# Optimization experiments

Hardware: AMD Instinct MI355X
Metric: run time of the kernel (lower is better)

## Reference

```python
import jax, jax.numpy as jnp
import numpy as np

DIM = 1024
INTER = 512
E = 32            # n_routed_experts
TOPK = 4          # n_activated_experts
GROUPS = 8        # n_expert_groups
TOPK_GROUPS = 4
SHARED_INTER = 2 * INTER  # n_shared_experts * moe_inter_dim
ROUTE_SCALE = 1.0
B, S = 8, 4096


def setup_inputs() -> dict:
    key = jax.random.key(0)
    ks = jax.random.split(key, 16)
    def xav(k, shape):
        fan_in, fan_out = shape[-2], shape[-1]
        lim = np.sqrt(6.0 / (fan_in + fan_out))
        return jax.random.uniform(k, shape, jnp.float32, -lim, lim)
    return {
        "x": jax.random.normal(ks[0], (B, S, DIM), jnp.float32),
        "gw": xav(ks[1], (DIM, E)),
        "gb": jnp.zeros((E,), jnp.float32),
        "w1": xav(ks[2], (E, DIM, INTER)),
        "b1": jnp.zeros((E, INTER), jnp.float32),
        "w3": xav(ks[3], (E, DIM, INTER)),
        "b3": jnp.zeros((E, INTER), jnp.float32),
        "w2": xav(ks[4], (E, INTER, DIM)),
        "b2": jnp.zeros((E, DIM), jnp.float32),
        "sw1": xav(ks[5], (DIM, SHARED_INTER)),
        "sb1": jnp.zeros((SHARED_INTER,), jnp.float32),
        "sw3": xav(ks[6], (DIM, SHARED_INTER)),
        "sb3": jnp.zeros((SHARED_INTER,), jnp.float32),
        "sw2": xav(ks[7], (SHARED_INTER, DIM)),
        "sb2": jnp.zeros((DIM,), jnp.float32),
    }


def _gate(xf, gw, gb):
    # scores: softmax over routed experts in fp32 (score_func='softmax')
    T = xf.shape[0]
    scores = jax.nn.softmax((xf @ gw + gb).astype(jnp.float32), axis=-1)  # [T, E]
    original_scores = scores
    # group-masked routing (n_expert_groups > 1)
    scores_g = scores.reshape(T, GROUPS, E // GROUPS)                     # [T, G, E/G]
    group_scores = jnp.sum(jax.lax.top_k(scores_g, 2)[0], axis=-1)        # [T, G]
    gidx = jax.lax.top_k(group_scores, TOPK_GROUPS)[1]                    # [T, topk_groups]
    keep = jnp.zeros((T, GROUPS), bool).at[jnp.arange(T)[:, None], gidx].set(True)
    masked = jnp.where(keep[:, :, None], scores_g, -jnp.inf).reshape(T, E)
    indices = jax.lax.top_k(masked, TOPK)[1]                              # [T, topk]
    weights = jnp.take_along_axis(original_scores, indices, axis=1) * ROUTE_SCALE
    return weights.astype(xf.dtype), indices


def reference(x, gw, gb, w1, b1, w3, b3, w2, b2, sw1, sb1, sw3, sb3, sw2, sb2):
    shape = x.shape
    xf = x.reshape(-1, DIM)                                               # [T, dim]
    T = xf.shape[0]
    weights, indices = _gate(xf, gw, gb)
    # dense combine weights [T, E]: w_e(t) = routing weight if expert e chosen for t else 0
    cw = jnp.zeros((T, E), xf.dtype).at[jnp.arange(T)[:, None], indices].add(weights)
    # scan over experts: y += w_e * SwiGLU_e(x). Zero weight -> zero contribution,
    # identical math to the masked dispatch/scatter-add in the torch code.
    def body(y, p):
        w1e, b1e, w3e, b3e, w2e, b2e, we = p
        h = jax.nn.silu(xf @ w1e + b1e) * (xf @ w3e + b3e)                # [T, inter]
        return y + we[:, None] * (h @ w2e + b2e), None
    y0 = jnp.zeros_like(xf)
    y, _ = jax.lax.scan(body, y0, (w1, b1, w3, b3, w2, b2, cw.T))
    # shared experts MLP (SwiGLU)
    z = (jax.nn.silu(xf @ sw1 + sb1) * (xf @ sw3 + sb3)) @ sw2 + sb2
    return (y + z).reshape(shape)
```

## Files before the change

kernel.cpp:

```cpp
#include <hip/hip_runtime.h>
#include <stdint.h>

#define DIM_    1024
#define INTER_  512

typedef short bf16x4 __attribute__((ext_vector_type(4)));
typedef short bf16x8 __attribute__((ext_vector_type(8)));
typedef float f32x4  __attribute__((ext_vector_type(4)));

__device__ __forceinline__ unsigned short f2bf(float f) {
  union { float f; unsigned u; } v; v.f = f;
  return (unsigned short)((v.u + 0x7FFFu + ((v.u >> 16) & 1u)) >> 16);
}
__device__ __forceinline__ unsigned f2bf2(float a, float b) {
  union { float f; unsigned u; } va, vb; va.f = a; vb.f = b;
  unsigned ra = (va.u + 0x7FFFu + ((va.u >> 16) & 1u)) >> 16;
  unsigned rb = (vb.u + 0x7FFFu + ((vb.u >> 16) & 1u)) >> 16;
  return ra | (rb << 16);
}
__device__ __forceinline__ float bfhi(unsigned u) {
  union { unsigned u; float f; } v; v.u = u & 0xffff0000u; return v.f;
}
__device__ __forceinline__ float bflo(unsigned u) {
  union { unsigned u; float f; } v; v.u = u << 16; return v.f;
}

__device__ __forceinline__ void gl16(const void* g, void* l) {
  __builtin_amdgcn_global_load_lds(
      (const __attribute__((address_space(1))) unsigned int*)g,
      (__attribute__((address_space(3))) unsigned int*)l, 16, 0, 0);
}

__global__ __launch_bounds__(256) void gate_kernel(
    const float* __restrict__ x, const float* __restrict__ gw,
    const float* __restrict__ gb, int* __restrict__ idx, float* __restrict__ wts,
    unsigned short* __restrict__ xb) {
  __shared__ double s_sc[4][32];
  __shared__ double s_gs[4][8];
  const int wid = threadIdx.x >> 6, lane = threadIdx.x & 63;
  const int t = blockIdx.x * 4 + wid;
  {
    const float* xrow = x + (size_t)t * DIM_ + lane * 16;
    unsigned short* xbrow = xb + (size_t)t * DIM_ + lane * 16;
    float4 f0 = *(const float4*)(xrow);
    float4 f1 = *(const float4*)(xrow + 4);
    float4 f2v = *(const float4*)(xrow + 8);
    float4 f3v = *(const float4*)(xrow + 12);
    uint4 o0, o1;
    o0.x = f2bf2(f0.x, f0.y);  o0.y = f2bf2(f0.z, f0.w);
    o0.z = f2bf2(f1.x, f1.y);  o0.w = f2bf2(f1.z, f1.w);
    o1.x = f2bf2(f2v.x, f2v.y); o1.y = f2bf2(f2v.z, f2v.w);
    o1.z = f2bf2(f3v.x, f3v.y); o1.w = f2bf2(f3v.z, f3v.w);
    *(uint4*)(xbrow) = o0;
    *(uint4*)(xbrow + 8) = o1;
  }
  const int e = lane & 31, half = lane >> 5;
  const float* xr  = x  + (size_t)t * DIM_ + half * 512;
  const float* gwp = gw + (size_t)half * 512 * 32 + e;
  double a0 = 0, a1 = 0, a2 = 0, a3 = 0;
  for (int k = 0; k < 512; k += 4) {
    float4 xv = *(const float4*)(xr + k);
    a0 += (double)xv.x * (double)gwp[(k + 0) * 32];
    a1 += (double)xv.y * (double)gwp[(k + 1) * 32];
    a2 += (double)xv.z * (double)gwp[(k + 2) * 32];
    a3 += (double)xv.w * (double)gwp[(k + 3) * 32];
  }
  double lg = (a0 + a1) + (a2 + a3);
  lg += __shfl_xor(lg, 32);
  lg += (double)gb[e];
  double m = lg;
  #pragma unroll
  for (int d = 1; d < 32; d <<= 1) m = fmax(m, __shfl_xor(m, d));
  double ex = exp(lg - m);
  double ssum = ex;
  #pragma unroll
  for (int d = 1; d < 32; d <<= 1) ssum += __shfl_xor(ssum, d);
  double sc = ex / ssum;
  double p  = __shfl_xor(sc, 1);
  double m1 = fmax(sc, p), n1 = fmin(sc, p);
  double m2 = __shfl_xor(m1, 2), n2 = __shfl_xor(n1, 2);
  double gs = (m1 >= m2) ? (m1 + fmax(n1, m2)) : (m2 + fmax(n2, m1));
  if (lane < 32) {
    s_sc[wid][e] = sc;
    if ((e & 3) == 0) s_gs[wid][e >> 2] = gs;
  }
  __syncthreads();
  if (lane == 0) {
    unsigned kmask = 0;
    for (int it = 0; it < 4; ++it) {
      int bg = 0; double bv = -1.0;
      for (int g = 0; g < 8; ++g)
        if (!((kmask >> g) & 1u) && s_gs[wid][g] > bv) { bv = s_gs[wid][g]; bg = g; }
      kmask |= 1u << bg;
    }
    unsigned umask = 0;
    for (int slot = 0; slot < 4; ++slot) {
      int be = 0; double bv = -1.0;
      for (int ee = 0; ee < 32; ++ee)
        if (((kmask >> (ee >> 2)) & 1u) && !((umask >> ee) & 1u) && s_sc[wid][ee] > bv) {
          bv = s_sc[wid][ee]; be = ee;
        }
      umask |= 1u << be;
      idx[t * 4 + slot] = be;
      wts[t * 4 + slot] = (float)bv;
    }
  }
}

__global__ __launch_bounds__(256) void count_kernel(const int* __restrict__ idx,
                                                    int* __restrict__ meta) {
  __shared__ int h[32];
  int tid = threadIdx.x;
  if (tid < 32) h[tid] = 0;
  __syncthreads();
  atomicAdd(&h[idx[blockIdx.x * 256 + tid]], 1);
  __syncthreads();
  if (tid < 32 && h[tid]) atomicAdd(&meta[tid], h[tid]);
}

__global__ void scan_kernel(int* __restrict__ meta) {
  int lane = threadIdx.x & 63;
  if (lane < 32) {
    int c = meta[lane];
    int pre = c;
    #pragma unroll
    for (int d = 1; d < 32; d <<= 1) { int t = __shfl_up(pre, d); if (lane >= d) pre += t; }
    int excl = pre - c;
    meta[64 + lane] = excl;
    meta[32 + lane] = excl;
    int nt = (c + 127) >> 7;
    int ntp = nt;
    #pragma unroll
    for (int d = 1; d < 32; d <<= 1) { int t = __shfl_up(ntp, d); if (lane >= d) ntp += t; }
    int ntExcl = ntp - nt;
    for (int k = 0; k < nt; ++k) { meta[128 + ntExcl + k] = lane; meta[1184 + ntExcl + k] = k << 7; }
    if (lane == 31) { meta[96] = excl + c; meta[97] = ntExcl + nt; }
  }
}

__global__ __launch_bounds__(256) void scatter_kernel(
    const int* __restrict__ idx, int* __restrict__ meta,
    int* __restrict__ tok, int* __restrict__ inv) {
  int i = blockIdx.x * 256 + threadIdx.x;
  int lane = threadIdx.x & 63;
  int e = idx[i];
  unsigned long long m = ~0ull;
  #pragma unroll
  for (int b = 0; b < 5; ++b) {
    unsigned long long vote = __ballot((e >> b) & 1);
    m &= ((e >> b) & 1) ? vote : ~vote;
  }
  int leader = __ffsll((long long)m) - 1;
  int rank = __popcll(m & ((1ull << lane) - 1));
  int base = 0;
  if (lane == leader) base = atomicAdd(&meta[32 + e], (int)__popcll(m));
  base = __shfl(base, leader);
  int p = base + rank;
  tok[p] = i >> 2;
  inv[i] = p;
}

__global__ __launch_bounds__(256) void repack_kernel(
    const float* __restrict__ src, unsigned short* __restrict__ dst,
    int K, int N, int tilesPerMat) {
  const int w = blockIdx.x * 4 + (threadIdx.x >> 6);
  const int j = threadIdx.x & 63;
  const int e = w / tilesPerMat, rem = w % tilesPerMat;
  const int kSteps = K >> 5;
  const int nt = rem / kSteps, kq = rem % kSteps;
  const float* s = src + (size_t)e * K * N + (size_t)(kq * 32) * N + nt * 64 + j;
  float v[32];
  #pragma unroll
  for (int kk = 0; kk < 32; ++kk) v[kk] = s[(size_t)kk * N];
  char* d = (char*)dst + (size_t)w * 4096 + j * 64;
  const int sz = (j & 3) ^ ((j >> 2) & 3);
  #pragma unroll
  for (int q = 0; q < 4; ++q) {
    int o = (q ^ sz) * 8;
    uint4 tv;
    tv.x = f2bf2(v[o + 0], v[o + 1]);
    tv.y = f2bf2(v[o + 2], v[o + 3]);
    tv.z = f2bf2(v[o + 4], v[o + 5]);
    tv.w = f2bf2(v[o + 6], v[o + 7]);
    *(uint4*)(d + q * 16) = tv;
  }
}

__global__ __launch_bounds__(256) void s1_kernel(
    const unsigned short* __restrict__ xb, const unsigned short* __restrict__ b1i,
    const unsigned short* __restrict__ b3i, const float* __restrict__ sb1,
    const float* __restrict__ sb3, unsigned short* __restrict__ Hs) {
  __shared__ char lds[32768];
  const int n0 = blockIdx.x * 64;
  const int m0 = blockIdx.y * 128;
  const int tid = threadIdx.x, lane = tid & 63, wave = tid >> 6;
  const int wm = wave >> 1, wn = wave & 1;

  const int r0 = tid >> 2, s0 = tid & 3;
  const int vrw = (r0 & 3) ^ ((r0 >> 2) & 1);
  const char* a0 = (const char*)xb + (size_t)(m0 + r0) * 2048 + ((s0 ^ vrw) << 4);
  const char* a1 = (const char*)xb + (size_t)(m0 + r0 + 64) * 2048 + ((s0 ^ vrw) << 4);
  const char* b1p = (const char*)b1i + (size_t)(blockIdx.x * 32) * 4096 + tid * 16;
  const char* b3p = (const char*)b3i + (size_t)(blockIdx.x * 32) * 4096 + tid * 16;

  const int g = lane >> 4;
  const int vfr = (lane & 3) ^ ((lane >> 2) & 1);
  const int aro = (wm * 64 + (lane & 15)) * 64 + ((g ^ vfr) << 4);
  int bofs[2];
  #pragma unroll
  for (int ni = 0; ni < 2; ++ni) {
    int j = wn * 32 + ni * 16 + (lane & 15);
    int sz = (j & 3) ^ ((j >> 2) & 3);
    bofs[ni] = j * 64 + ((g ^ sz) << 4);
  }

  f32x4 acc1[4][2], acc3[4][2];
  const f32x4 zz = {0.f, 0.f, 0.f, 0.f};
  #pragma unroll
  for (int mi = 0; mi < 4; ++mi)
    #pragma unroll
    for (int ni = 0; ni < 2; ++ni) { acc1[mi][ni] = zz; acc3[mi][ni] = zz; }

  auto stage = [&](int buf, int kq) {
    char* b = lds + buf * 16384;
    gl16(a0 + kq * 64, b + wave * 1024);
    gl16(a1 + kq * 64, b + 4096 + wave * 1024);
    gl16(b1p + (size_t)kq * 4096, b + 8192 + wave * 1024);
    gl16(b3p + (size_t)kq * 4096, b + 12288 + wave * 1024);
  };
  stage(0, 0);
  __syncthreads();
  int cur = 0;
  for (int kq = 0; kq < 32; ++kq) {
    if (kq + 1 < 32) stage(cur ^ 1, kq + 1);
    char* cb = lds + cur * 16384;
    bf16x8 af[4];
    #pragma unroll
    for (int mi = 0; mi < 4; ++mi) af[mi] = *(const bf16x8*)(cb + aro + mi * 1024);
    #pragma unroll
    for (int ni = 0; ni < 2; ++ni) {
      bf16x8 bv = *(const bf16x8*)(cb + 8192 + bofs[ni]);
      #pragma unroll
      for (int mi = 0; mi < 4; ++mi)
        acc1[mi][ni] = __builtin_amdgcn_mfma_f32_16x16x32_bf16(af[mi], bv, acc1[mi][ni], 0, 0, 0);
      bf16x8 bv3 = *(const bf16x8*)(cb + 12288 + bofs[ni]);
      #pragma unroll
      for (int mi = 0; mi < 4; ++mi)
        acc3[mi][ni] = __builtin_amdgcn_mfma_f32_16x16x32_bf16(af[mi], bv3, acc3[mi][ni], 0, 0, 0);
    }
    __syncthreads();
    cur ^= 1;
  }
  #pragma unroll
  for (int ni = 0; ni < 2; ++ni) {
    int col = n0 + wn * 32 + ni * 16 + (lane & 15);
    float bb1 = sb1[col], bb3 = sb3[col];
    #pragma unroll
    for (int mi = 0; mi < 4; ++mi) {
      int rb = wm * 64 + mi * 16 + ((lane >> 4) << 2);
      #pragma unroll
      for (int r = 0; r < 4; ++r) {
        int row = m0 + rb + r;
        float v1 = acc1[mi][ni][r] + bb1;
        float v3 = acc3[mi][ni][r] + bb3;
        float h = (v1 / (1.f + __expf(-v1))) * v3;
        Hs[(size_t)row * 1024 + col] = f2bf(h);
      }
    }
  }
}

__global__ __launch_bounds__(256) void s2_kernel(
    const unsigned short* __restrict__ Hs, const unsigned short* __restrict__ b2i,
    const float* __restrict__ sb2, float* __restrict__ out) {
  __shared__ char lds[32768];
  const int n0 = blockIdx.x * 128;
  const int m0 = blockIdx.y * 128;
  const int tid = threadIdx.x, lane = tid & 63, wave = tid >> 6;
  const int wm = wave >> 1, wn = wave & 1;

  const int r0 = tid >> 2, s0 = tid & 3;
  const int vrw = (r0 & 3) ^ ((r0 >> 2) & 1);
  const char* a0 = (const char*)Hs + (size_t)(m0 + r0) * 2048 + ((s0 ^ vrw) << 4);
  const char* a1 = (const char*)Hs + (size_t)(m0 + r0 + 64) * 2048 + ((s0 ^ vrw) << 4);
  const char* bp0 = (const char*)b2i + (size_t)((blockIdx.x * 2 + 0) * 32) * 4096 + tid * 16;
  const char* bp1 = (const char*)b2i + (size_t)((blockIdx.x * 2 + 1) * 32) * 4096 + tid * 16;

  const int g = lane >> 4;
  const int vfr = (lane & 3) ^ ((lane >> 2) & 1);
  const int aro = (wm * 64 + (lane & 15)) * 64 + ((g ^ vfr) << 4);
  int bofs[4];
  #pragma unroll
  for (int ni = 0; ni < 4; ++ni) {
    int j = wn * 64 + ni * 16 + (lane & 15);
    int sz = (j & 3) ^ ((j >> 2) & 3);
    bofs[ni] = 8192 + (j >> 6) * 4096 + (j & 63) * 64 + ((g ^ sz) << 4);
  }
  f32x4 acc[4][4];
  const f32x4 zz = {0.f, 0.f, 0.f, 0.f};
  #pragma unroll
  for (int mi = 0; mi < 4; ++mi)
    #pragma unroll
    for (int ni = 0; ni < 4; ++ni) acc[mi][ni] = zz;

  auto stage = [&](int buf, int kq) {
    char* b = lds + buf * 16384;
    gl16(a0 + kq * 64, b + wave * 1024);
    gl16(a1 + kq * 64, b + 4096 + wave * 1024);
    gl16(bp0 + (size_t)kq * 4096, b + 8192 + wave * 1024);
    gl16(bp1 + (size_t)kq * 4096, b + 12288 + wave * 1024);
  };
  stage(0, 0);
  __syncthreads();
  int cur = 0;
  for (int kq = 0; kq < 32; ++kq) {
    if (kq + 1 < 32) stage(cur ^ 1, kq + 1);
    char* cb = lds + cur * 16384;
    bf16x8 af[4];
    #pragma unroll
    for (int mi = 0; mi < 4; ++mi) af[mi] = *(const bf16x8*)(cb + aro + mi * 1024);
    #pragma unroll
    for (int ni = 0; ni < 4; ++ni) {
      bf16x8 bv = *(const bf16x8*)(cb + bofs[ni]);
      #pragma unroll
      for (int mi = 0; mi < 4; ++mi)
        acc[mi][ni] = __builtin_amdgcn_mfma_f32_16x16x32_bf16(af[mi], bv, acc[mi][ni], 0, 0, 0);
    }
    __syncthreads();
    cur ^= 1;
  }
  #pragma unroll
  for (int ni = 0; ni < 4; ++ni) {
    int col = n0 + wn * 64 + ni * 16 + (lane & 15);
    float bb = sb2[col];
    #pragma unroll
    for (int mi = 0; mi < 4; ++mi) {
      int rb = m0 + wm * 64 + mi * 16 + ((lane >> 4) << 2);
      #pragma unroll
      for (int r = 0; r < 4; ++r)
        out[(size_t)(rb + r) * 1024 + col] = acc[mi][ni][r] + bb;
    }
  }
}

__global__ __launch_bounds__(256) void g1_kernel(
    const unsigned short* __restrict__ xb, const unsigned short* __restrict__ w1i,
    const unsigned short* __restrict__ w3i, const float* __restrict__ b1,
    const float* __restrict__ b3, const int* __restrict__ tok,
    const int* __restrict__ meta, unsigned short* __restrict__ H) {
  __shared__ char lds[32768];
  if ((int)blockIdx.y >= meta[97]) return;
  const int e = meta[128 + blockIdx.y], m0 = meta[1184 + blockIdx.y];
  const int off_e = meta[64 + e], nrem = meta[e] - m0;
  const int n0 = blockIdx.x * 64;
  const int tid = threadIdx.x, lane = tid & 63, wave = tid >> 6;
  const int wm = wave >> 1, wn = wave & 1;

  const int r0 = tid >> 2, s0 = tid & 3;
  const int vrw = (r0 & 3) ^ ((r0 >> 2) & 1);
  int tr0 = tok[off_e + m0 + ((r0 < nrem) ? r0 : 0)];
  int tr1 = tok[off_e + m0 + ((r0 + 64 < nrem) ? r0 + 64 : 0)];
  const char* a0 = (const char*)xb + (size_t)tr0 * 2048 + ((s0 ^ vrw) << 4);
  const char* a1 = (const char*)xb + (size_t)tr1 * 2048 + ((s0 ^ vrw) << 4);
  const char* b1p = (const char*)w1i + (size_t)((e * 8 + blockIdx.x) * 32) * 4096 + tid * 16;
  const char* b3p = (const char*)w3i + (size_t)((e * 8 + blockIdx.x) * 32) * 4096 + tid * 16;

  const int g = lane >> 4;
  const int vfr = (lane & 3) ^ ((lane >> 2) & 1);
  const int aro = (wm * 64 + (lane & 15)) * 64 + ((g ^ vfr) << 4);
  int bofs[2];
  #pragma unroll
  for (int ni = 0; ni < 2; ++ni) {
    int j = wn * 32 + ni * 16 + (lane & 15);
    int sz = (j & 3) ^ ((j >> 2) & 3);
    bofs[ni] = j * 64 + ((g ^ sz) << 4);
  }

  f32x4 acc1[4][2], acc3[4][2];
  const f32x4 zz = {0.f, 0.f, 0.f, 0.f};
  #pragma unroll
  for (int mi = 0; mi < 4; ++mi)
    #pragma unroll
    for (int ni = 0; ni < 2; ++ni) { acc1[mi][ni] = zz; acc3[mi][ni] = zz; }

  auto stage = [&](int buf, int kq) {
    char* b = lds + buf * 16384;
    gl16(a0 + kq * 64, b + wave * 1024);
    gl16(a1 + kq * 64, b + 4096 + wave * 1024);
    gl16(b1p + (size_t)kq * 4096, b + 8192 + wave * 1024);
    gl16(b3p + (size_t)kq * 4096, b + 12288 + wave * 1024);
  };
  stage(0, 0);
  __syncthreads();
  int cur = 0;
  for (int kq = 0; kq < 32; ++kq) {
    if (kq + 1 < 32) stage(cur ^ 1, kq + 1);
    char* cb = lds + cur * 16384;
    bf16x8 af[4];
    #pragma unroll
    for (int mi = 0; mi < 4; ++mi) af[mi] = *(const bf16x8*)(cb + aro + mi * 1024);
    #pragma unroll
    for (int ni = 0; ni < 2; ++ni) {
      bf16x8 bv = *(const bf16x8*)(cb + 8192 + bofs[ni]);
      #pragma unroll
      for (int mi = 0; mi < 4; ++mi)
        acc1[mi][ni] = __builtin_amdgcn_mfma_f32_16x16x32_bf16(af[mi], bv, acc1[mi][ni], 0, 0, 0);
      bf16x8 bv3 = *(const bf16x8*)(cb + 12288 + bofs[ni]);
      #pragma unroll
      for (int mi = 0; mi < 4; ++mi)
        acc3[mi][ni] = __builtin_amdgcn_mfma_f32_16x16x32_bf16(af[mi], bv3, acc3[mi][ni], 0, 0, 0);
    }
    __syncthreads();
    cur ^= 1;
  }
  #pragma unroll
  for (int ni = 0; ni < 2; ++ni) {
    int col = n0 + wn * 32 + ni * 16 + (lane & 15);
    float bb1 = b1[e * 512 + col], bb3 = b3[e * 512 + col];
    #pragma unroll
    for (int mi = 0; mi < 4; ++mi) {
      int rb = wm * 64 + mi * 16 + ((lane >> 4) << 2);
      #pragma unroll
      for (int r = 0; r < 4; ++r) {
        int row = rb + r;
        if (row < nrem) {
          float v1 = acc1[mi][ni][r] + bb1;
          float v3 = acc3[mi][ni][r] + bb3;
          float h = (v1 / (1.f + __expf(-v1))) * v3;
          H[(size_t)(off_e + m0 + row) * 512 + col] = f2bf(h);
        }
      }
    }
  }
}

__global__ __launch_bounds__(256) void g2_kernel(
    const unsigned short* __restrict__ H, const unsigned short* __restrict__ w2i,
    const float* __restrict__ b2, const int* __restrict__ meta,
    unsigned short* __restrict__ Y, int cbase) {
  __shared__ char lds[32768];
  if ((int)blockIdx.y >= meta[97]) return;
  const int e = meta[128 + blockIdx.y], m0 = meta[1184 + blockIdx.y];
  const int off_e = meta[64 + e], nrem = meta[e] - m0;
  const int n0 = cbase + blockIdx.x * 128;
  const int tid = threadIdx.x, lane = tid & 63, wave = tid >> 6;
  const int wm = wave >> 1, wn = wave & 1;

  const int r0 = tid >> 2, s0 = tid & 3;
  const int vrw = (r0 & 3) ^ ((r0 >> 2) & 1);
  const char* a0 = (const char*)H + (size_t)(off_e + m0 + ((r0 < nrem) ? r0 : 0)) * 1024 + ((s0 ^ vrw) << 4);
  const char* a1 = (const char*)H + (size_t)(off_e + m0 + ((r0 + 64 < nrem) ? r0 + 64 : 0)) * 1024 + ((s0 ^ vrw) << 4);
  const int ntb = n0 >> 6;
  const char* bp0 = (const char*)w2i + (size_t)((e * 16 + ntb + 0) * 16) * 4096 + tid * 16;
  const char* bp1 = (const char*)w2i + (size_t)((e * 16 + ntb + 1) * 16) * 4096 + tid * 16;

  const int g = lane >> 4;
  const int vfr = (lane & 3) ^ ((lane >> 2) & 1);
  const int aro = (wm * 64 + (lane & 15)) * 64 + ((g ^ vfr) << 4);
  int bofs[4];
  #pragma unroll
  for (int ni = 0; ni < 4; ++ni) {
    int j = wn * 64 + ni * 16 + (lane & 15);
    int sz = (j & 3) ^ ((j >> 2) & 3);
    bofs[ni] = 8192 + (j >> 6) * 4096 + (j & 63) * 64 + ((g ^ sz) << 4);
  }
  f32x4 acc[4][4];
  const f32x4 zz = {0.f, 0.f, 0.f, 0.f};
  #pragma unroll
  for (int mi = 0; mi < 4; ++mi)
    #pragma unroll
    for (int ni = 0; ni < 4; ++ni) acc[mi][ni] = zz;

  auto stage = [&](int buf, int kq) {
    char* b = lds + buf * 16384;
    gl16(a0 + kq * 64, b + wave * 1024);
    gl16(a1 + kq * 64, b + 4096 + wave * 1024);
    gl16(bp0 + (size_t)kq * 4096, b + 8192 + wave * 1024);
    gl16(bp1 + (size_t)kq * 4096, b + 12288 + wave * 1024);
  };
  stage(0, 0);
  __syncthreads();
  int cur = 0;
  for (int kq = 0; kq < 16; ++kq) {
    if (kq + 1 < 16) stage(cur ^ 1, kq + 1);
    char* cb = lds + cur * 16384;
    bf16x8 af[4];
    #pragma unroll
    for (int mi = 0; mi < 4; ++mi) af[mi] = *(const bf16x8*)(cb + aro + mi * 1024);
    #pragma unroll
    for (int ni = 0; ni < 4; ++ni) {
      bf16x8 bv = *(const bf16x8*)(cb + bofs[ni]);
      #pragma unroll
      for (int mi = 0; mi < 4; ++mi)
        acc[mi][ni] = __builtin_amdgcn_mfma_f32_16x16x32_bf16(af[mi], bv, acc[mi][ni], 0, 0, 0);
    }
    __syncthreads();
    cur ^= 1;
  }
  #pragma unroll
  for (int ni = 0; ni < 4; ++ni) {
    int col = n0 + wn * 64 + ni * 16 + (lane & 15);
    float bb = b2[e * 1024 + col];
    int ycol = col - cbase;
    #pragma unroll
    for (int mi = 0; mi < 4; ++mi) {
      int rb = wm * 64 + mi * 16 + ((lane >> 4) << 2);
      #pragma unroll
      for (int r = 0; r < 4; ++r) {
        int row = rb + r;
        if (row < nrem)
          Y[(size_t)(off_e + m0 + row) * 512 + ycol] = f2bf(acc[mi][ni][r] + bb);
      }
    }
  }
}

__global__ __launch_bounds__(256) void combine_kernel(
    const unsigned short* __restrict__ Y, const int* __restrict__ inv,
    const float* __restrict__ wts, float* __restrict__ out, int cbase) {
  int t = blockIdx.x * 2 + (threadIdx.x >> 7);
  int c = (threadIdx.x & 127) * 4;
  int4 iv = *(const int4*)(inv + t * 4);
  float4 wv = *(const float4*)(wts + t * 4);
  float* op = out + (size_t)t * 1024 + cbase + c;
  float4 o = *(float4*)op;
  uint2 u;
  u = *(const uint2*)(Y + (size_t)iv.x * 512 + c);
  o.x += wv.x * bflo(u.x); o.y += wv.x * bfhi(u.x);
  o.z += wv.x * bflo(u.y); o.w += wv.x * bfhi(u.y);
  u = *(const uint2*)(Y + (size_t)iv.y * 512 + c);
  o.x += wv.y * bflo(u.x); o.y += wv.y * bfhi(u.x);
  o.z += wv.y * bflo(u.y); o.w += wv.y * bfhi(u.y);
  u = *(const uint2*)(Y + (size_t)iv.z * 512 + c);
  o.x += wv.z * bflo(u.x); o.y += wv.z * bfhi(u.x);
  o.z += wv.z * bflo(u.y); o.w += wv.z * bfhi(u.y);
  u = *(const uint2*)(Y + (size_t)iv.w * 512 + c);
  o.x += wv.w * bflo(u.x); o.y += wv.w * bfhi(u.x);
  o.z += wv.w * bflo(u.y); o.w += wv.w * bfhi(u.y);
  *(float4*)op = o;
}

extern "C" void kernel_launch(void* const* d_in, const int* in_sizes, int n_in,
                              void* d_out, int out_size, void* d_ws, size_t ws_size,
                              hipStream_t stream) {
  const float* x   = (const float*)d_in[0];
  const float* gw  = (const float*)d_in[1];
  const float* gb  = (const float*)d_in[2];
  const float* w1  = (const float*)d_in[3];
  const float* b1  = (const float*)d_in[4];
  const float* w3  = (const float*)d_in[5];
  const float* b3  = (const float*)d_in[6];
  const float* w2  = (const float*)d_in[7];
  const float* b2  = (const float*)d_in[8];
  const float* sw1 = (const float*)d_in[9];
  const float* sb1 = (const float*)d_in[10];
  const float* sw3 = (const float*)d_in[11];
  const float* sb3 = (const float*)d_in[12];
  const float* sw2 = (const float*)d_in[13];
  const float* sb2 = (const float*)d_in[14];
  float* out = (float*)d_out;
  char* ws = (char*)d_ws;

  const size_t OFF_XB   = 134217728;
  const size_t OFF_W1I  = 201326592;
  const size_t OFF_W3I  = 234881024;
  const size_t OFF_W2I  = 268435456;
  const size_t OFF_SW1I = 301989888;
  const size_t OFF_SW3I = 304087040;
  const size_t OFF_SW2I = 306184192;
  const size_t OFF_IDX  = 308281344;
  const size_t OFF_WTS  = 308805632;
  const size_t OFF_TOK  = 309329920;
  const size_t OFF_INV  = 309854208;
  const size_t OFF_META = 310378496;
  if (ws_size < OFF_META + 8960) return;

  unsigned short* H    = (unsigned short*)ws;
  unsigned short* xb   = (unsigned short*)(ws + OFF_XB);
  unsigned short* Yb   = (unsigned short*)(ws + OFF_XB);
  unsigned short* w1i  = (unsigned short*)(ws + OFF_W1I);
  unsigned short* w3i  = (unsigned short*)(ws + OFF_W3I);
  unsigned short* w2i  = (unsigned short*)(ws + OFF_W2I);
  unsigned short* sw1i = (unsigned short*)(ws + OFF_SW1I);
  unsigned short* sw3i = (unsigned short*)(ws + OFF_SW3I);
  unsigned short* sw2i = (unsigned short*)(ws + OFF_SW2I);
  int*   idx  = (int*)(ws + OFF_IDX);
  float* wts  = (float*)(ws + OFF_WTS);
  int*   tokl = (int*)(ws + OFF_TOK);
  int*   inv  = (int*)(ws + OFF_INV);
  int*   meta = (int*)(ws + OFF_META);

  hipMemsetAsync(meta, 0, 128, stream);
  gate_kernel<<<dim3(8192), dim3(256), 0, stream>>>(x, gw, gb, idx, wts, xb);
  count_kernel<<<dim3(512), dim3(256), 0, stream>>>(idx, meta);
  scan_kernel<<<dim3(1), dim3(64), 0, stream>>>(meta);
  scatter_kernel<<<dim3(512), dim3(256), 0, stream>>>(idx, meta, tokl, inv);
  repack_kernel<<<dim3(2048), dim3(256), 0, stream>>>(w1, w1i, 1024, 512, 256);
  repack_kernel<<<dim3(2048), dim3(256), 0, stream>>>(w3, w3i, 1024, 512, 256);
  repack_kernel<<<dim3(2048), dim3(256), 0, stream>>>(w2, w2i, 512, 1024, 256);
  repack_kernel<<<dim3(128), dim3(256), 0, stream>>>(sw1, sw1i, 1024, 1024, 512);
  repack_kernel<<<dim3(128), dim3(256), 0, stream>>>(sw3, sw3i, 1024, 1024, 512);
  repack_kernel<<<dim3(128), dim3(256), 0, stream>>>(sw2, sw2i, 1024, 1024, 512);
  s1_kernel<<<dim3(16, 256), dim3(256), 0, stream>>>(xb, sw1i, sw3i, sb1, sb3, H);
  s2_kernel<<<dim3(8, 256), dim3(256), 0, stream>>>(H, sw2i, sb2, out);
  g1_kernel<<<dim3(8, 1056), dim3(256), 0, stream>>>(xb, w1i, w3i, b1, b3, tokl, meta, H);
  g2_kernel<<<dim3(4, 1056), dim3(256), 0, stream>>>(H, w2i, b2, meta, Yb, 0);
  combine_kernel<<<dim3(16384), dim3(256), 0, stream>>>(Yb, inv, wts, out, 0);
  g2_kernel<<<dim3(4, 1056), dim3(256), 0, stream>>>(H, w2i, b2, meta, Yb, 512);
  combine_kernel<<<dim3(16384), dim3(256), 0, stream>>>(Yb, inv, wts, out, 512);
}
```

Before: 1.605 ms.

## Interleave w1/w3 weight images and switch GEMMs to single-buffered K=64 stages

A new repack13 kernel interleaves w1 and w3 columns in 16-wide groups into one bf16 image, so the gated GEMMs read a single B stream through a common 4x4 MFMA tile layout. All four GEMM kernels now share one macro body that stages a 64-wide K slice per iteration (twice the previous depth) into a single LDS buffer, with a barrier before and after each stage. This halves the number of loop iterations and barriers and merges two repack launches into one. In exchange the previous double-buffered prefetch is gone, so global loads no longer overlap with MFMA work inside a block.

```diff
diff --git a/kernel.cpp b/kernel.cpp
--- a/kernel.cpp
+++ b/kernel.cpp
@@ -186,85 +186,120 @@
   }
 }
 
+__global__ __launch_bounds__(256) void repack13_kernel(
+    const float* __restrict__ src1, const float* __restrict__ src3,
+    unsigned short* __restrict__ dst, int K, int N, int jtTiles) {
+  const int w = blockIdx.x * 4 + (threadIdx.x >> 6);
+  const int j = threadIdx.x & 63;
+  const int kSteps = K >> 5;
+  const int tpm = jtTiles * kSteps;
+  const int e = w / tpm, rem = w % tpm;
+  const int jt = rem / kSteps, kq = rem % kSteps;
+  const int jg = jt * 64 + j;
+  const int c = ((jg >> 5) << 4) + (jg & 15);
+  const float* s = (((jg >> 4) & 1) ? src3 : src1)
+                 + (size_t)e * K * N + (size_t)(kq * 32) * N + c;
+  float v[32];
+  #pragma unroll
+  for (int kk = 0; kk < 32; ++kk) v[kk] = s[(size_t)kk * N];
+  char* d = (char*)dst + (size_t)w * 4096 + j * 64;
+  const int sz = (j & 3) ^ ((j >> 2) & 3);
+  #pragma unroll
+  for (int q = 0; q < 4; ++q) {
+    int o = (q ^ sz) * 8;
+    uint4 tv;
+    tv.x = f2bf2(v[o + 0], v[o + 1]);
+    tv.y = f2bf2(v[o + 2], v[o + 3]);
+    tv.z = f2bf2(v[o + 4], v[o + 5]);
+    tv.w = f2bf2(v[o + 6], v[o + 7]);
+    *(uint4*)(d + q * 16) = tv;
+  }
+}
+
+
+#define GEMM_PRE()                                                            \
+  const int tid = threadIdx.x, lane = tid & 63, wave = tid >> 6;              \
+  const int wm = wave >> 1, wn = wave & 1;                                    \
+  const int f = lane & 15, g = lane >> 4;                                     \
+  const int rr = ((tid >> 6) << 4) + ((tid & 63) >> 2);                       \
+  const int sl = tid & 3;                                                     \
+  const int soff = ((sl ^ ((rr & 3) ^ ((rr >> 2) & 1))) << 4);                \
+  const int vfr = (f & 3) ^ ((f >> 2) & 1);                                   \
+  const int aro = (wm * 64 + f) * 64 + ((g ^ vfr) << 4);                      \
+  int bofs[4];                                                                \
+  _Pragma("unroll")                                                           \
+  for (int ni = 0; ni < 4; ++ni) {                                            \
+    int j = wn * 64 + ni * 16 + f;                                            \
+    int jl = j & 63;                                                          \
+    int szv = (jl & 3) ^ ((jl >> 2) & 3);                                     \
+    bofs[ni] = 16384 + (j >> 6) * 4096 + jl * 64 + ((g ^ szv) << 4);          \
+  }                                                                           \
+  f32x4 acc[4][4];                                                            \
+  const f32x4 zz = {0.f, 0.f, 0.f, 0.f};                                      \
+  _Pragma("unroll")                                                           \
+  for (int mi = 0; mi < 4; ++mi)                                              \
+    _Pragma("unroll")                                                         \
+    for (int ni = 0; ni < 4; ++ni) acc[mi][ni] = zz;
+
+#define GEMM_STAGE(ks)                                                        \
+  gl16(pA0 + (ks) * 128,        lds + wave * 1024);                           \
+  gl16(pA1 + (ks) * 128,        lds + 4096 + wave * 1024);                    \
+  gl16(pA0 + (ks) * 128 + 64,   lds + 8192 + wave * 1024);                    \
+  gl16(pA1 + (ks) * 128 + 64,   lds + 12288 + wave * 1024);                   \
+  gl16(bimg0 + (size_t)(ks) * 8192,        lds + 16384 + wave * 1024);        \
+  gl16(bimg1 + (size_t)(ks) * 8192,        lds + 20480 + wave * 1024);        \
+  gl16(bimg0 + (size_t)(ks) * 8192 + 4096, lds + 24576 + wave * 1024);        \
+  gl16(bimg1 + (size_t)(ks) * 8192 + 4096, lds + 28672 + wave * 1024);
+
+#define GEMM_COMPUTE()                                                        \
+  _Pragma("unroll")                                                           \
+  for (int kk = 0; kk < 2; ++kk) {                                            \
+    bf16x8 af[4], bf[4];                                                      \
+    _Pragma("unroll")                                                         \
+    for (int mi = 0; mi < 4; ++mi)                                            \
+      af[mi] = *(const bf16x8*)(lds + kk * 8192 + aro + mi * 1024);           \
+    _Pragma("unroll")                                                         \
+    for (int ni = 0; ni < 4; ++ni)                                            \
+      bf[ni] = *(const bf16x8*)(lds + kk * 8192 + bofs[ni]);                  \
+    _Pragma("unroll")                                                         \
+    for (int ni = 0; ni < 4; ++ni)                                            \
+      _Pragma("unroll")                                                       \
+      for (int mi = 0; mi < 4; ++mi)                                          \
+        acc[mi][ni] = __builtin_amdgcn_mfma_f32_16x16x32_bf16(                \
+            af[mi], bf[ni], acc[mi][ni], 0, 0, 0);                            \
+  }
+
 __global__ __launch_bounds__(256) void s1_kernel(
-    const unsigned short* __restrict__ xb, const unsigned short* __restrict__ b1i,
-    const unsigned short* __restrict__ b3i, const float* __restrict__ sb1,
-    const float* __restrict__ sb3, unsigned short* __restrict__ Hs) {
+    const unsigned short* __restrict__ xb, const unsigned short* __restrict__ w13,
+    const float* __restrict__ sb1, const float* __restrict__ sb3,
+    unsigned short* __restrict__ Hs) {
   __shared__ char lds[32768];
-  const int n0 = blockIdx.x * 64;
   const int m0 = blockIdx.y * 128;
-  const int tid = threadIdx.x, lane = tid & 63, wave = tid >> 6;
-  const int wm = wave >> 1, wn = wave & 1;
-
-  const int r0 = tid >> 2, s0 = tid & 3;
-  const int vrw = (r0 & 3) ^ ((r0 >> 2) & 1);
-  const char* a0 = (const char*)xb + (size_t)(m0 + r0) * 2048 + ((s0 ^ vrw) << 4);
-  const char* a1 = (const char*)xb + (size_t)(m0 + r0 + 64) * 2048 + ((s0 ^ vrw) << 4);
-  const char* b1p = (const char*)b1i + (size_t)(blockIdx.x * 32) * 4096 + tid * 16;
-  const char* b3p = (const char*)b3i + (size_t)(blockIdx.x * 32) * 4096 + tid * 16;
-
-  const int g = lane >> 4;
-  const int vfr = (lane & 3) ^ ((lane >> 2) & 1);
-  const int aro = (wm * 64 + (lane & 15)) * 64 + ((g ^ vfr) << 4);
-  int bofs[2];
-  #pragma unroll
-  for (int ni = 0; ni < 2; ++ni) {
-    int j = wn * 32 + ni * 16 + (lane & 15);
-    int sz = (j & 3) ^ ((j >> 2) & 3);
-    bofs[ni] = j * 64 + ((g ^ sz) << 4);
-  }
-
-  f32x4 acc1[4][2], acc3[4][2];
-  const f32x4 zz = {0.f, 0.f, 0.f, 0.f};
-  #pragma unroll
-  for (int mi = 0; mi < 4; ++mi)
-    #pragma unroll
-    for (int ni = 0; ni < 2; ++ni) { acc1[mi][ni] = zz; acc3[mi][ni] = zz; }
-
-  auto stage = [&](int buf, int kq) {
-    char* b = lds + buf * 16384;
-    gl16(a0 + kq * 64, b + wave * 1024);
-    gl16(a1 + kq * 64, b + 4096 + wave * 1024);
-    gl16(b1p + (size_t)kq * 4096, b + 8192 + wave * 1024);
-    gl16(b3p + (size_t)kq * 4096, b + 12288 + wave * 1024);
-  };
-  stage(0, 0);
-  __syncthreads();
-  int cur = 0;
-  for (int kq = 0; kq < 32; ++kq) {
-    if (kq + 1 < 32) stage(cur ^ 1, kq + 1);
-    char* cb = lds + cur * 16384;
-    bf16x8 af[4];
-    #pragma unroll
-    for (int mi = 0; mi < 4; ++mi) af[mi] = *(const bf16x8*)(cb + aro + mi * 1024);
-    #pragma unroll
-    for (int ni = 0; ni < 2; ++ni) {
-      bf16x8 bv = *(const bf16x8*)(cb + 8192 + bofs[ni]);
-      #pragma unroll
-      for (int mi = 0; mi < 4; ++mi)
-        acc1[mi][ni] = __builtin_amdgcn_mfma_f32_16x16x32_bf16(af[mi], bv, acc1[mi][ni], 0, 0, 0);
-      bf16x8 bv3 = *(const bf16x8*)(cb + 12288 + bofs[ni]);
-      #pragma unroll
-      for (int mi = 0; mi < 4; ++mi)
-        acc3[mi][ni] = __builtin_amdgcn_mfma_f32_16x16x32_bf16(af[mi], bv3, acc3[mi][ni], 0, 0, 0);
-    }
-    __syncthreads();
-    cur ^= 1;
-  }
-  #pragma unroll
-  for (int ni = 0; ni < 2; ++ni) {
-    int col = n0 + wn * 32 + ni * 16 + (lane & 15);
+  GEMM_PRE();
+  const char* pA0 = (const char*)xb + (size_t)(m0 + rr) * 2048 + soff;
+  const char* pA1 = (const char*)xb + (size_t)(m0 + rr + 64) * 2048 + soff;
+  const char* bimg0 = (const char*)w13 + (size_t)((blockIdx.x * 2 + 0) * 32) * 4096 + tid * 16;
+  const char* bimg1 = (const char*)w13 + (size_t)((blockIdx.x * 2 + 1) * 32) * 4096 + tid * 16;
+  for (int ks = 0; ks < 16; ++ks) {
+    __syncthreads();
+    GEMM_STAGE(ks);
+    __syncthreads();
+    GEMM_COMPUTE();
+  }
+  const int bx64 = blockIdx.x * 64;
+  #pragma unroll
+  for (int p = 0; p < 2; ++p) {
+    int col = bx64 + (wn * 2 + p) * 16 + f;
     float bb1 = sb1[col], bb3 = sb3[col];
     #pragma unroll
     for (int mi = 0; mi < 4; ++mi) {
-      int rb = wm * 64 + mi * 16 + ((lane >> 4) << 2);
+      int rb = wm * 64 + mi * 16 + (g << 2);
       #pragma unroll
       for (int r = 0; r < 4; ++r) {
-        int row = m0 + rb + r;
-        float v1 = acc1[mi][ni][r] + bb1;
-        float v3 = acc3[mi][ni][r] + bb3;
+        float v1 = acc[mi][2 * p][r] + bb1;
+        float v3 = acc[mi][2 * p + 1][r] + bb3;
         float h = (v1 / (1.f + __expf(-v1))) * v3;
-        Hs[(size_t)row * 1024 + col] = f2bf(h);
+        Hs[(size_t)(m0 + rb + r) * 1024 + col] = f2bf(h);
       }
     }
   }
@@ -274,68 +309,26 @@
     const unsigned short* __restrict__ Hs, const unsigned short* __restrict__ b2i,
     const float* __restrict__ sb2, float* __restrict__ out) {
   __shared__ char lds[32768];
+  const int m0 = blockIdx.y * 128;
   const int n0 = blockIdx.x * 128;
-  const int m0 = blockIdx.y * 128;
-  const int tid = threadIdx.x, lane = tid & 63, wave = tid >> 6;
-  const int wm = wave >> 1, wn = wave & 1;
-
-  const int r0 = tid >> 2, s0 = tid & 3;
-  const int vrw = (r0 & 3) ^ ((r0 >> 2) & 1);
-  const char* a0 = (const char*)Hs + (size_t)(m0 + r0) * 2048 + ((s0 ^ vrw) << 4);
-  const char* a1 = (const char*)Hs + (size_t)(m0 + r0 + 64) * 2048 + ((s0 ^ vrw) << 4);
-  const char* bp0 = (const char*)b2i + (size_t)((blockIdx.x * 2 + 0) * 32) * 4096 + tid * 16;
-  const char* bp1 = (const char*)b2i + (size_t)((blockIdx.x * 2 + 1) * 32) * 4096 + tid * 16;
-
-  const int g = lane >> 4;
-  const int vfr = (lane & 3) ^ ((lane >> 2) & 1);
-  const int aro = (wm * 64 + (lane & 15)) * 64 + ((g ^ vfr) << 4);
-  int bofs[4];
+  GEMM_PRE();
+  const char* pA0 = (const char*)Hs + (size_t)(m0 + rr) * 2048 + soff;
+  const char* pA1 = (const char*)Hs + (size_t)(m0 + rr + 64) * 2048 + soff;
+  const char* bimg0 = (const char*)b2i + (size_t)((blockIdx.x * 2 + 0) * 32) * 4096 + tid * 16;
+  const char* bimg1 = (const char*)b2i + (size_t)((blockIdx.x * 2 + 1) * 32) * 4096 + tid * 16;
+  for (int ks = 0; ks < 16; ++ks) {
+    __syncthreads();
+    GEMM_STAGE(ks);
+    __syncthreads();
+    GEMM_COMPUTE();
+  }
   #pragma unroll
   for (int ni = 0; ni < 4; ++ni) {
-    int j = wn * 64 + ni * 16 + (lane & 15);
-    int sz = (j & 3) ^ ((j >> 2) & 3);
-    bofs[ni] = 8192 + (j >> 6) * 4096 + (j & 63) * 64 + ((g ^ sz) << 4);
-  }
-  f32x4 acc[4][4];
-  const f32x4 zz = {0.f, 0.f, 0.f, 0.f};
-  #pragma unroll
-  for (int mi = 0; mi < 4; ++mi)
-    #pragma unroll
-    for (int ni = 0; ni < 4; ++ni) acc[mi][ni] = zz;
-
-  auto stage = [&](int buf, int kq) {
-    char* b = lds + buf * 16384;
-    gl16(a0 + kq * 64, b + wave * 1024);
-    gl16(a1 + kq * 64, b + 4096 + wave * 1024);
-    gl16(bp0 + (size_t)kq * 4096, b + 8192 + wave * 1024);
-    gl16(bp1 + (size_t)kq * 4096, b + 12288 + wave * 1024);
-  };
-  stage(0, 0);
-  __syncthreads();
-  int cur = 0;
-  for (int kq = 0; kq < 32; ++kq) {
-    if (kq + 1 < 32) stage(cur ^ 1, kq + 1);
-    char* cb = lds + cur * 16384;
-    bf16x8 af[4];
-    #pragma unroll
-    for (int mi = 0; mi < 4; ++mi) af[mi] = *(const bf16x8*)(cb + aro + mi * 1024);
-    #pragma unroll
-    for (int ni = 0; ni < 4; ++ni) {
-      bf16x8 bv = *(const bf16x8*)(cb + bofs[ni]);
-      #pragma unroll
-      for (int mi = 0; mi < 4; ++mi)
-        acc[mi][ni] = __builtin_amdgcn_mfma_f32_16x16x32_bf16(af[mi], bv, acc[mi][ni], 0, 0, 0);
-    }
-    __syncthreads();
-    cur ^= 1;
-  }
-  #pragma unroll
-  for (int ni = 0; ni < 4; ++ni) {
-    int col = n0 + wn * 64 + ni * 16 + (lane & 15);
+    int col = n0 + wn * 64 + ni * 16 + f;
     float bb = sb2[col];
     #pragma unroll
     for (int mi = 0; mi < 4; ++mi) {
-      int rb = m0 + wm * 64 + mi * 16 + ((lane >> 4) << 2);
+      int rb = m0 + wm * 64 + mi * 16 + (g << 2);
       #pragma unroll
       for (int r = 0; r < 4; ++r)
         out[(size_t)(rb + r) * 1024 + col] = acc[mi][ni][r] + bb;
@@ -344,88 +337,41 @@
 }
 
 __global__ __launch_bounds__(256) void g1_kernel(
-    const unsigned short* __restrict__ xb, const unsigned short* __restrict__ w1i,
-    const unsigned short* __restrict__ w3i, const float* __restrict__ b1,
-    const float* __restrict__ b3, const int* __restrict__ tok,
-    const int* __restrict__ meta, unsigned short* __restrict__ H) {
+    const unsigned short* __restrict__ xb, const unsigned short* __restrict__ w13,
+    const float* __restrict__ b1, const float* __restrict__ b3,
+    const int* __restrict__ tok, const int* __restrict__ meta,
+    unsigned short* __restrict__ H) {
   __shared__ char lds[32768];
   if ((int)blockIdx.y >= meta[97]) return;
   const int e = meta[128 + blockIdx.y], m0 = meta[1184 + blockIdx.y];
   const int off_e = meta[64 + e], nrem = meta[e] - m0;
-  const int n0 = blockIdx.x * 64;
-  const int tid = threadIdx.x, lane = tid & 63, wave = tid >> 6;
-  const int wm = wave >> 1, wn = wave & 1;
-
-  const int r0 = tid >> 2, s0 = tid & 3;
-  const int vrw = (r0 & 3) ^ ((r0 >> 2) & 1);
-  int tr0 = tok[off_e + m0 + ((r0 < nrem) ? r0 : 0)];
-  int tr1 = tok[off_e + m0 + ((r0 + 64 < nrem) ? r0 + 64 : 0)];
-  const char* a0 = (const char*)xb + (size_t)tr0 * 2048 + ((s0 ^ vrw) << 4);
-  const char* a1 = (const char*)xb + (size_t)tr1 * 2048 + ((s0 ^ vrw) << 4);
-  const char* b1p = (const char*)w1i + (size_t)((e * 8 + blockIdx.x) * 32) * 4096 + tid * 16;
-  const char* b3p = (const char*)w3i + (size_t)((e * 8 + blockIdx.x) * 32) * 4096 + tid * 16;
-
-  const int g = lane >> 4;
-  const int vfr = (lane & 3) ^ ((lane >> 2) & 1);
-  const int aro = (wm * 64 + (lane & 15)) * 64 + ((g ^ vfr) << 4);
-  int bofs[2];
-  #pragma unroll
-  for (int ni = 0; ni < 2; ++ni) {
-    int j = wn * 32 + ni * 16 + (lane & 15);
-    int sz = (j & 3) ^ ((j >> 2) & 3);
-    bofs[ni] = j * 64 + ((g ^ sz) << 4);
-  }
-
-  f32x4 acc1[4][2], acc3[4][2];
-  const f32x4 zz = {0.f, 0.f, 0.f, 0.f};
-  #pragma unroll
-  for (int mi = 0; mi < 4; ++mi)
-    #pragma unroll
-    for (int ni = 0; ni < 2; ++ni) { acc1[mi][ni] = zz; acc3[mi][ni] = zz; }
-
-  auto stage = [&](int buf, int kq) {
-    char* b = lds + buf * 16384;
-    gl16(a0 + kq * 64, b + wave * 1024);
-    gl16(a1 + kq * 64, b + 4096 + wave * 1024);
-    gl16(b1p + (size_t)kq * 4096, b + 8192 + wave * 1024);
-    gl16(b3p + (size_t)kq * 4096, b + 12288 + wave * 1024);
-  };
-  stage(0, 0);
-  __syncthreads();
-  int cur = 0;
-  for (int kq = 0; kq < 32; ++kq) {
-    if (kq + 1 < 32) stage(cur ^ 1, kq + 1);
-    char* cb = lds + cur * 16384;
-    bf16x8 af[4];
-    #pragma unroll
-    for (int mi = 0; mi < 4; ++mi) af[mi] = *(const bf16x8*)(cb + aro + mi * 1024);
-    #pragma unroll
-    for (int ni = 0; ni < 2; ++ni) {
-      bf16x8 bv = *(const bf16x8*)(cb + 8192 + bofs[ni]);
-      #pragma unroll
-      for (int mi = 0; mi < 4; ++mi)
-        acc1[mi][ni] = __builtin_amdgcn_mfma_f32_16x16x32_bf16(af[mi], bv, acc1[mi][ni], 0, 0, 0);
-      bf16x8 bv3 = *(const bf16x8*)(cb + 12288 + bofs[ni]);
-      #pragma unroll
-      for (int mi = 0; mi < 4; ++mi)
-        acc3[mi][ni] = __builtin_amdgcn_mfma_f32_16x16x32_bf16(af[mi], bv3, acc3[mi][ni], 0, 0, 0);
-    }
-    __syncthreads();
-    cur ^= 1;
-  }
-  #pragma unroll
-  for (int ni = 0; ni < 2; ++ni) {
-    int col = n0 + wn * 32 + ni * 16 + (lane & 15);
+  GEMM_PRE();
+  int tr0 = tok[off_e + m0 + ((rr < nrem) ? rr : 0)];
+  int tr1 = tok[off_e + m0 + ((rr + 64 < nrem) ? rr + 64 : 0)];
+  const char* pA0 = (const char*)xb + (size_t)tr0 * 2048 + soff;
+  const char* pA1 = (const char*)xb + (size_t)tr1 * 2048 + soff;
+  const char* bimg0 = (const char*)w13 + (size_t)((e * 16 + blockIdx.x * 2 + 0) * 32) * 4096 + tid * 16;
+  const char* bimg1 = (const char*)w13 + (size_t)((e * 16 + blockIdx.x * 2 + 1) * 32) * 4096 + tid * 16;
+  for (int ks = 0; ks < 16; ++ks) {
+    __syncthreads();
+    GEMM_STAGE(ks);
+    __syncthreads();
+    GEMM_COMPUTE();
+  }
+  const int bx64 = blockIdx.x * 64;
+  #pragma unroll
+  for (int p = 0; p < 2; ++p) {
+    int col = bx64 + (wn * 2 + p) * 16 + f;
     float bb1 = b1[e * 512 + col], bb3 = b3[e * 512 + col];
     #pragma unroll
     for (int mi = 0; mi < 4; ++mi) {
-      int rb = wm * 64 + mi * 16 + ((lane >> 4) << 2);
+      int rb = wm * 64 + mi * 16 + (g << 2);
       #pragma unroll
       for (int r = 0; r < 4; ++r) {
         int row = rb + r;
         if (row < nrem) {
-          float v1 = acc1[mi][ni][r] + bb1;
-          float v3 = acc3[mi][ni][r] + bb3;
+          float v1 = acc[mi][2 * p][r] + bb1;
+          float v3 = acc[mi][2 * p + 1][r] + bb3;
           float h = (v1 / (1.f + __expf(-v1))) * v3;
           H[(size_t)(off_e + m0 + row) * 512 + col] = f2bf(h);
         }
@@ -443,68 +389,26 @@
   const int e = meta[128 + blockIdx.y], m0 = meta[1184 + blockIdx.y];
   const int off_e = meta[64 + e], nrem = meta[e] - m0;
   const int n0 = cbase + blockIdx.x * 128;
-  const int tid = threadIdx.x, lane = tid & 63, wave = tid >> 6;
-  const int wm = wave >> 1, wn = wave & 1;
-
-  const int r0 = tid >> 2, s0 = tid & 3;
-  const int vrw = (r0 & 3) ^ ((r0 >> 2) & 1);
-  const char* a0 = (const char*)H + (size_t)(off_e + m0 + ((r0 < nrem) ? r0 : 0)) * 1024 + ((s0 ^ vrw) << 4);
-  const char* a1 = (const char*)H + (size_t)(off_e + m0 + ((r0 + 64 < nrem) ? r0 + 64 : 0)) * 1024 + ((s0 ^ vrw) << 4);
-  const int ntb = n0 >> 6;
-  const char* bp0 = (const char*)w2i + (size_t)((e * 16 + ntb + 0) * 16) * 4096 + tid * 16;
-  const char* bp1 = (const char*)w2i + (size_t)((e * 16 + ntb + 1) * 16) * 4096 + tid * 16;
-
-  const int g = lane >> 4;
-  const int vfr = (lane & 3) ^ ((lane >> 2) & 1);
-  const int aro = (wm * 64 + (lane & 15)) * 64 + ((g ^ vfr) << 4);
-  int bofs[4];
+  GEMM_PRE();
+  const char* pA0 = (const char*)H + (size_t)(off_e + m0 + ((rr < nrem) ? rr : 0)) * 1024 + soff;
+  const char* pA1 = (const char*)H + (size_t)(off_e + m0 + ((rr + 64 < nrem) ? rr + 64 : 0)) * 1024 + soff;
+  const int ntb = (n0 >> 6);
+  const char* bimg0 = (const char*)w2i + (size_t)((e * 16 + ntb + 0) * 16) * 4096 + tid * 16;
+  const char* bimg1 = (const char*)w2i + (size_t)((e * 16 + ntb + 1) * 16) * 4096 + tid * 16;
+  for (int ks = 0; ks < 8; ++ks) {
+    __syncthreads();
+    GEMM_STAGE(ks);
+    __syncthreads();
+    GEMM_COMPUTE();
+  }
   #pragma unroll
   for (int ni = 0; ni < 4; ++ni) {
-    int j = wn * 64 + ni * 16 + (lane & 15);
-    int sz = (j & 3) ^ ((j >> 2) & 3);
-    bofs[ni] = 8192 + (j >> 6) * 4096 + (j & 63) * 64 + ((g ^ sz) << 4);
-  }
-  f32x4 acc[4][4];
-  const f32x4 zz = {0.f, 0.f, 0.f, 0.f};
-  #pragma unroll
-  for (int mi = 0; mi < 4; ++mi)
-    #pragma unroll
-    for (int ni = 0; ni < 4; ++ni) acc[mi][ni] = zz;
-
-  auto stage = [&](int buf, int kq) {
-    char* b = lds + buf * 16384;
-    gl16(a0 + kq * 64, b + wave * 1024);
-    gl16(a1 + kq * 64, b + 4096 + wave * 1024);
-    gl16(bp0 + (size_t)kq * 4096, b + 8192 + wave * 1024);
-    gl16(bp1 + (size_t)kq * 4096, b + 12288 + wave * 1024);
-  };
-  stage(0, 0);
-  __syncthreads();
-  int cur = 0;
-  for (int kq = 0; kq < 16; ++kq) {
-    if (kq + 1 < 16) stage(cur ^ 1, kq + 1);
-    char* cb = lds + cur * 16384;
-    bf16x8 af[4];
-    #pragma unroll
-    for (int mi = 0; mi < 4; ++mi) af[mi] = *(const bf16x8*)(cb + aro + mi * 1024);
-    #pragma unroll
-    for (int ni = 0; ni < 4; ++ni) {
-      bf16x8 bv = *(const bf16x8*)(cb + bofs[ni]);
-      #pragma unroll
-      for (int mi = 0; mi < 4; ++mi)
-        acc[mi][ni] = __builtin_amdgcn_mfma_f32_16x16x32_bf16(af[mi], bv, acc[mi][ni], 0, 0, 0);
-    }
-    __syncthreads();
-    cur ^= 1;
-  }
-  #pragma unroll
-  for (int ni = 0; ni < 4; ++ni) {
-    int col = n0 + wn * 64 + ni * 16 + (lane & 15);
+    int col = n0 + wn * 64 + ni * 16 + f;
     float bb = b2[e * 1024 + col];
     int ycol = col - cbase;
     #pragma unroll
     for (int mi = 0; mi < 4; ++mi) {
-      int rb = wm * 64 + mi * 16 + ((lane >> 4) << 2);
+      int rb = wm * 64 + mi * 16 + (g << 2);
       #pragma unroll
       for (int r = 0; r < 4; ++r) {
         int row = rb + r;
@@ -562,11 +466,9 @@
   char* ws = (char*)d_ws;
 
   const size_t OFF_XB   = 134217728;
-  const size_t OFF_W1I  = 201326592;
-  const size_t OFF_W3I  = 234881024;
+  const size_t OFF_W13I = 201326592;
   const size_t OFF_W2I  = 268435456;
-  const size_t OFF_SW1I = 301989888;
-  const size_t OFF_SW3I = 304087040;
+  const size_t OFF_S13I = 301989888;
   const size_t OFF_SW2I = 306184192;
   const size_t OFF_IDX  = 308281344;
   const size_t OFF_WTS  = 308805632;
@@ -578,11 +480,9 @@
   unsigned short* H    = (unsigned short*)ws;
   unsigned short* xb   = (unsigned short*)(ws + OFF_XB);
   unsigned short* Yb   = (unsigned short*)(ws + OFF_XB);
-  unsigned short* w1i  = (unsigned short*)(ws + OFF_W1I);
-  unsigned short* w3i  = (unsigned short*)(ws + OFF_W3I);
+  unsigned short* w13i = (unsigned short*)(ws + OFF_W13I);
   unsigned short* w2i  = (unsigned short*)(ws + OFF_W2I);
-  unsigned short* sw1i = (unsigned short*)(ws + OFF_SW1I);
-  unsigned short* sw3i = (unsigned short*)(ws + OFF_SW3I);
+  unsigned short* s13i = (unsigned short*)(ws + OFF_S13I);
   unsigned short* sw2i = (unsigned short*)(ws + OFF_SW2I);
   int*   idx  = (int*)(ws + OFF_IDX);
   float* wts  = (float*)(ws + OFF_WTS);
@@ -595,15 +495,13 @@
   count_kernel<<<dim3(512), dim3(256), 0, stream>>>(idx, meta);
   scan_kernel<<<dim3(1), dim3(64), 0, stream>>>(meta);
   scatter_kernel<<<dim3(512), dim3(256), 0, stream>>>(idx, meta, tokl, inv);
-  repack_kernel<<<dim3(2048), dim3(256), 0, stream>>>(w1, w1i, 1024, 512, 256);
-  repack_kernel<<<dim3(2048), dim3(256), 0, stream>>>(w3, w3i, 1024, 512, 256);
+  repack13_kernel<<<dim3(4096), dim3(256), 0, stream>>>(w1, w3, w13i, 1024, 512, 16);
   repack_kernel<<<dim3(2048), dim3(256), 0, stream>>>(w2, w2i, 512, 1024, 256);
-  repack_kernel<<<dim3(128), dim3(256), 0, stream>>>(sw1, sw1i, 1024, 1024, 512);
-  repack_kernel<<<dim3(128), dim3(256), 0, stream>>>(sw3, sw3i, 1024, 1024, 512);
+  repack13_kernel<<<dim3(256), dim3(256), 0, stream>>>(sw1, sw3, s13i, 1024, 1024, 32);
   repack_kernel<<<dim3(128), dim3(256), 0, stream>>>(sw2, sw2i, 1024, 1024, 512);
-  s1_kernel<<<dim3(16, 256), dim3(256), 0, stream>>>(xb, sw1i, sw3i, sb1, sb3, H);
+  s1_kernel<<<dim3(16, 256), dim3(256), 0, stream>>>(xb, s13i, sb1, sb3, H);
   s2_kernel<<<dim3(8, 256), dim3(256), 0, stream>>>(H, sw2i, sb2, out);
-  g1_kernel<<<dim3(8, 1056), dim3(256), 0, stream>>>(xb, w1i, w3i, b1, b3, tokl, meta, H);
+  g1_kernel<<<dim3(8, 1056), dim3(256), 0, stream>>>(xb, w13i, b1, b3, tokl, meta, H);
   g2_kernel<<<dim3(4, 1056), dim3(256), 0, stream>>>(H, w2i, b2, meta, Yb, 0);
   combine_kernel<<<dim3(16384), dim3(256), 0, stream>>>(Yb, inv, wts, out, 0);
   g2_kernel<<<dim3(4, 1056), dim3(256), 0, stream>>>(H, w2i, b2, meta, Yb, 512);
```

New measurement: 1.667 ms. 1.04x slower.
